# Kernel optimization log

Measured on AMD Instinct MI355X. Metric: run time of the kernel, lower is better.

The kernel has to match this reference:

```python
import jax, jax.numpy as jnp
import numpy as np
from jax import lax


def _pairwise_dist(a, b):
    # a: (T, D), b: (T, D) -> (T, T) Euclidean distances via GEMM trick
    a2 = jnp.sum(a * a, axis=-1)
    b2 = jnp.sum(b * b, axis=-1)
    sq = a2[:, None] + b2[None, :] - 2.0 * (a @ b.T)
    return jnp.sqrt(jnp.maximum(sq, 1e-12))


def _frechet(seq1, seq2):
    cost = _pairwise_dist(seq1, seq2)  # (T, T)
    ca0 = lax.cummax(cost[0])          # first row boundary: running max

    def row_step(prev, cost_row):
        # prev: ca[i-1, :]; cost_row: cost[i, :]
        c0 = jnp.maximum(prev[0], cost_row[0])  # first-column boundary

        def col_step(left, x):
            c, up, diag = x
            val = jnp.maximum(c, jnp.minimum(jnp.minimum(up, left), diag))
            return val, val

        _, rest = lax.scan(col_step, c0, (cost_row[1:], prev[1:], prev[:-1]))
        cur = jnp.concatenate([c0[None], rest])
        return cur, None

    final_row, _ = lax.scan(row_step, ca0, cost[1:])
    return final_row[-1]


def setup_inputs() -> dict:
    key = jax.random.key(0)
    k1, k2 = jax.random.split(key)
    B, T, D = 32, 1024, 64
    pred = jax.random.normal(k1, (B, T, D), dtype=jnp.float32)
    targ = jax.random.normal(k2, (B, T, D), dtype=jnp.float32)
    return {"pred": pred, "targ": targ}


def reference(pred, targ):
    dists = jax.vmap(_frechet)(pred, targ)  # (B,)
    return jnp.mean(dists)
```

## Files before the change

### kernel.cpp

```cpp
#include <hip/hip_runtime.h>
#include <hip/hip_bf16.h>

#define T_LEN 1024
#define D_DIM 64
#define BATCH 32

#define BM 64
#define BN 128

__global__ __launch_bounds__(256, 3) void cost_kernel(const float* __restrict__ pred,
                                                      const float* __restrict__ targ,
                                                      float* __restrict__ cost) {
    const int b = blockIdx.z;
    const float* P = pred + (size_t)b * T_LEN * D_DIM;
    const float* Tg = targ + (size_t)b * T_LEN * D_DIM;
    float* C = cost + (size_t)b * T_LEN * T_LEN;
    const int row0 = blockIdx.y * BM;
    const int col0 = blockIdx.x * BN;

    __shared__ __align__(16) float ps[BM][D_DIM + 4];
    __shared__ __align__(16) float ts[D_DIM][BN + 4];
    __shared__ float p2[BM], t2[BN];

    const int tid = threadIdx.x;

#pragma unroll
    for (int it = 0; it < 4; ++it) {
        int f = tid + 256 * it;
        int row = f >> 4;
        int kc = f & 15;
        float4 v = *(const float4*)(P + (size_t)(row0 + row) * D_DIM + 4 * kc);
        *(float4*)&ps[row][4 * kc] = v;
    }
#pragma unroll
    for (int it = 0; it < 8; ++it) {
        int f = tid + 256 * it;
        int col = f >> 4;
        int kc = f & 15;
        float4 w = *(const float4*)(Tg + (size_t)(col0 + col) * D_DIM + 4 * kc);
        ts[4 * kc + 0][col] = w.x;
        ts[4 * kc + 1][col] = w.y;
        ts[4 * kc + 2][col] = w.z;
        ts[4 * kc + 3][col] = w.w;
    }
    __syncthreads();

    if (tid < 64) {
        float s = 0.0f;
        const float4* pr = (const float4*)&ps[tid][0];
#pragma unroll
        for (int q = 0; q < 16; ++q) {
            float4 v = pr[q];
            s += v.x * v.x; s += v.y * v.y; s += v.z * v.z; s += v.w * v.w;
        }
        p2[tid] = s;
    } else if (tid < 192) {
        int c = tid - 64;
        float s = 0.0f;
#pragma unroll
        for (int k = 0; k < 64; ++k) { float x = ts[k][c]; s += x * x; }
        t2[c] = s;
    }
    __syncthreads();

    const int tx = tid & 31;
    const int ty = tid >> 5;
    const int r0 = 8 * ty, c0 = 4 * tx;

    float acc[8][4];
#pragma unroll
    for (int i = 0; i < 8; ++i)
#pragma unroll
        for (int j = 0; j < 4; ++j) acc[i][j] = 0.0f;

#pragma unroll
    for (int k4 = 0; k4 < 16; ++k4) {
        float4 b0 = *(const float4*)&ts[4 * k4 + 0][c0];
        float4 b1 = *(const float4*)&ts[4 * k4 + 1][c0];
        float4 b2 = *(const float4*)&ts[4 * k4 + 2][c0];
        float4 b3 = *(const float4*)&ts[4 * k4 + 3][c0];
#pragma unroll
        for (int i = 0; i < 8; ++i) {
            float4 a = *(const float4*)&ps[r0 + i][4 * k4];
            acc[i][0] += a.x * b0.x; acc[i][1] += a.x * b0.y; acc[i][2] += a.x * b0.z; acc[i][3] += a.x * b0.w;
            acc[i][0] += a.y * b1.x; acc[i][1] += a.y * b1.y; acc[i][2] += a.y * b1.z; acc[i][3] += a.y * b1.w;
            acc[i][0] += a.z * b2.x; acc[i][1] += a.z * b2.y; acc[i][2] += a.z * b2.z; acc[i][3] += a.z * b2.w;
            acc[i][0] += a.w * b3.x; acc[i][1] += a.w * b3.y; acc[i][2] += a.w * b3.z; acc[i][3] += a.w * b3.w;
        }
    }

    float4 tt = *(const float4*)&t2[c0];
#pragma unroll
    for (int i = 0; i < 8; ++i) {
        float pa = p2[r0 + i];
        float4 o;
        o.x = sqrtf(fmaxf(pa + tt.x - 2.0f * acc[i][0], 1e-12f));
        o.y = sqrtf(fmaxf(pa + tt.y - 2.0f * acc[i][1], 1e-12f));
        o.z = sqrtf(fmaxf(pa + tt.z - 2.0f * acc[i][2], 1e-12f));
        o.w = sqrtf(fmaxf(pa + tt.w - 2.0f * acc[i][3], 1e-12f));
        *(float4*)(C + (size_t)(row0 + r0 + i) * T_LEN + (col0 + c0)) = o;
    }
}

#define RD 12

__device__ __forceinline__ void gl_lds16(const float* g, void* l) {
    __builtin_amdgcn_global_load_lds(
        (const __attribute__((address_space(1))) unsigned int*)(const void*)g,
        (__attribute__((address_space(3))) unsigned int*)l, 16, 0, 0);
}

__device__ __forceinline__ float4 lds_read_b128(unsigned off) {
    float4 r;
    asm volatile("ds_read_b128 %0, %1" : "=v"(r) : "v"(off));
    return r;
}

__global__ __launch_bounds__(64) void dp_kernel(const float* __restrict__ cost,
                                                float* __restrict__ out) {
    const int b = blockIdx.x;
    const int t = threadIdx.x;
    const float INF = __builtin_inff();
    const float* C = cost + (size_t)b * T_LEN * T_LEN + 16 * t;

    __shared__ __align__(16) float4 ring[RD][4][64];

    const unsigned ring_base =
        (unsigned)(size_t)(__attribute__((address_space(3))) void*)&ring[0][0][0];
    const unsigned my_off = ring_base + 16u * (unsigned)t;

    float prev[16];
#pragma unroll
    for (int j = 0; j < 16; ++j) prev[j] = INF;
    float right_out = INF;
    float diag_feed = INF;

#pragma unroll
    for (int d = 0; d < RD; ++d) {
        int r = d - t; r = r < 0 ? 0 : (r > T_LEN - 1 ? T_LEN - 1 : r);
        const float* src = C + (size_t)r * T_LEN;
#pragma unroll
        for (int q = 0; q < 4; ++q) gl_lds16(src + 4 * q, &ring[d][q][0]);
    }

    float4 rA0, rA1, rA2, rA3, rB0, rB1, rB2, rB3;
    asm volatile("s_waitcnt vmcnt(44)" ::: "memory");
    __builtin_amdgcn_sched_barrier(0);
    rA0 = lds_read_b128(my_off + 0);
    rA1 = lds_read_b128(my_off + 1024);
    rA2 = lds_read_b128(my_off + 2048);
    rA3 = lds_read_b128(my_off + 3072);

    const int S = T_LEN + 63;
    const int NCH = (S + RD - 1) / RD;
    int s = 0;

#define DP_STEP(C0, C1, C2, C3, N0, N1, N2, N3, USLOT)                        \
    {                                                                         \
        asm volatile("s_waitcnt lgkmcnt(0)" ::: "memory");                    \
        __builtin_amdgcn_sched_barrier(0);                                    \
        const int r = s - t;                                                  \
        float inc = __shfl_up(right_out, 1, 64);                              \
        float left = inc, diag = diag_feed;                                   \
        diag_feed = inc;                                                      \
        if (t == 0) { left = (r == 0) ? -INF : INF; diag = INF; }             \
        if (r >= 0 && r < T_LEN) {                                            \
            float cb[16] = {C0.x, C0.y, C0.z, C0.w, C1.x, C1.y, C1.z, C1.w,   \
                            C2.x, C2.y, C2.z, C2.w, C3.x, C3.y, C3.z, C3.w};  \
            _Pragma("unroll")                                                 \
            for (int j = 0; j < 16; ++j) {                                    \
                float c = cb[j];                                              \
                float up = prev[j];                                           \
                float v = fmaxf(c, fminf(fminf(up, diag), left));             \
                diag = up; left = v; prev[j] = v;                             \
            }                                                                 \
            right_out = left;                                                 \
        }                                                                     \
        __builtin_amdgcn_sched_barrier(0);                                    \
        asm volatile("s_waitcnt vmcnt(40)" ::: "memory");                     \
        __builtin_amdgcn_sched_barrier(0);                                    \
        {                                                                     \
            const unsigned nb = my_off + ((((USLOT) + 1) % RD) * 4096u);      \
            N0 = lds_read_b128(nb + 0);                                       \
            N1 = lds_read_b128(nb + 1024);                                    \
            N2 = lds_read_b128(nb + 2048);                                    \
            N3 = lds_read_b128(nb + 3072);                                    \
            int rn = s + RD - t;                                              \
            rn = rn < 0 ? 0 : (rn > T_LEN - 1 ? T_LEN - 1 : rn);              \
            const float* src = C + (size_t)rn * T_LEN;                        \
            gl_lds16(src + 0,  &ring[USLOT][0][0]);                           \
            gl_lds16(src + 4,  &ring[USLOT][1][0]);                           \
            gl_lds16(src + 8,  &ring[USLOT][2][0]);                           \
            gl_lds16(src + 12, &ring[USLOT][3][0]);                           \
        }                                                                     \
        ++s;                                                                  \
    }

    for (int chunk = 0; chunk < NCH; ++chunk) {
        DP_STEP(rA0, rA1, rA2, rA3, rB0, rB1, rB2, rB3, 0)
        DP_STEP(rB0, rB1, rB2, rB3, rA0, rA1, rA2, rA3, 1)
        DP_STEP(rA0, rA1, rA2, rA3, rB0, rB1, rB2, rB3, 2)
        DP_STEP(rB0, rB1, rB2, rB3, rA0, rA1, rA2, rA3, 3)
        DP_STEP(rA0, rA1, rA2, rA3, rB0, rB1, rB2, rB3, 4)
        DP_STEP(rB0, rB1, rB2, rB3, rA0, rA1, rA2, rA3, 5)
        DP_STEP(rA0, rA1, rA2, rA3, rB0, rB1, rB2, rB3, 6)
        DP_STEP(rB0, rB1, rB2, rB3, rA0, rA1, rA2, rA3, 7)
        DP_STEP(rA0, rA1, rA2, rA3, rB0, rB1, rB2, rB3, 8)
        DP_STEP(rB0, rB1, rB2, rB3, rA0, rA1, rA2, rA3, 9)
        DP_STEP(rA0, rA1, rA2, rA3, rB0, rB1, rB2, rB3, 10)
        DP_STEP(rB0, rB1, rB2, rB3, rA0, rA1, rA2, rA3, 11)
    }
#undef DP_STEP

    asm volatile("s_waitcnt vmcnt(0) lgkmcnt(0)" ::: "memory");
    if (t == 63) atomicAdd(out, prev[15] * (1.0f / (float)BATCH));
}

__global__ __launch_bounds__(64) void dp_fused_kernel(const float* __restrict__ pred,
                                                      const float* __restrict__ targ,
                                                      float* __restrict__ out) {
    const int b = blockIdx.x;
    const int t = threadIdx.x;
    const float INF = __builtin_inff();
    const float* P = pred + (size_t)b * T_LEN * D_DIM;
    const float* T = targ + (size_t)b * T_LEN * D_DIM + (size_t)(16 * t) * D_DIM;

    float prev[16];
#pragma unroll
    for (int j = 0; j < 16; ++j) prev[j] = INF;
    float right_out = INF;
    float diag_feed = INF;

    for (int s = 0; s < T_LEN + 63; s++) {
        int r = s - t;
        float inc = __shfl_up(right_out, 1, 64);
        float left = inc, diag = diag_feed;
        diag_feed = inc;
        if (t == 0) { left = (r == 0) ? -INF : INF; diag = INF; }
        if (r >= 0 && r < T_LEN) {
            float4 pr[16];
            const float4* pp = (const float4*)(P + (size_t)r * D_DIM);
#pragma unroll
            for (int q = 0; q < 16; q++) pr[q] = pp[q];
#pragma unroll
            for (int j = 0; j < 16; j++) {
                const float4* tp = (const float4*)(T + (size_t)j * D_DIM);
                float acc = 0.0f;
#pragma unroll
                for (int q = 0; q < 16; q++) {
                    float4 tv = tp[q];
                    float dx = pr[q].x - tv.x; acc += dx * dx;
                    float dy = pr[q].y - tv.y; acc += dy * dy;
                    float dz = pr[q].z - tv.z; acc += dz * dz;
                    float dw = pr[q].w - tv.w; acc += dw * dw;
                }
                float c = sqrtf(fmaxf(acc, 1e-12f));
                float up = prev[j];
                float v = fmaxf(c, fminf(fminf(up, diag), left));
                diag = up; left = v; prev[j] = v;
            }
            right_out = left;
        }
    }
    if (t == 63) atomicAdd(out, prev[15] * (1.0f / (float)BATCH));
}

extern "C" void kernel_launch(void* const* d_in, const int* in_sizes, int n_in,
                              void* d_out, int out_size, void* d_ws, size_t ws_size,
                              hipStream_t stream) {
    const float* pred = (const float*)d_in[0];
    const float* targ = (const float*)d_in[1];
    float* out = (float*)d_out;

    hipMemsetAsync(out, 0, sizeof(float) * out_size, stream);

    const size_t per_batch = (size_t)T_LEN * T_LEN * sizeof(float);
    int bpg = (int)(ws_size / per_batch);
    if (bpg > BATCH) bpg = BATCH;

    if (bpg >= 1) {
        float* cost = (float*)d_ws;
        for (int g0 = 0; g0 < BATCH; g0 += bpg) {
            int gb = (BATCH - g0) < bpg ? (BATCH - g0) : bpg;
            dim3 grid(T_LEN / BN, T_LEN / BM, gb);
            cost_kernel<<<grid, 256, 0, stream>>>(pred + (size_t)g0 * T_LEN * D_DIM,
                                                  targ + (size_t)g0 * T_LEN * D_DIM,
                                                  cost);
            dp_kernel<<<gb, 64, 0, stream>>>(cost, out);
        }
    } else {
        dp_fused_kernel<<<BATCH, 64, 0, stream>>>(pred, targ, out);
    }
}
```

Baseline: 342.5 us.

## Replace LDS ring prefetch with register pipeline and med3-based DP recurrence

The DP kernel no longer stages cost rows through an LDS ring buffer via global_load_lds. It now keeps an 8-deep register pipeline of direct global_load_dwordx4 loads, waiting with vmcnt. The inner recurrence is also reformulated: the up/diag terms are precomputed independently, and the serial dependency on left becomes a single fmed3 per element, which shortens the critical chain. The register pipeline costs many VGPRs, and the shallower prefetch depth may expose more memory latency.

```diff
diff --git a/kernel.cpp b/kernel.cpp
--- a/kernel.cpp
+++ b/kernel.cpp
@@ -102,19 +102,15 @@
     }
 }
 
-#define RD 12
-
-__device__ __forceinline__ void gl_lds16(const float* g, void* l) {
-    __builtin_amdgcn_global_load_lds(
-        (const __attribute__((address_space(1))) unsigned int*)(const void*)g,
-        (__attribute__((address_space(3))) unsigned int*)l, 16, 0, 0);
-}
-
-__device__ __forceinline__ float4 lds_read_b128(unsigned off) {
-    float4 r;
-    asm volatile("ds_read_b128 %0, %1" : "=v"(r) : "v"(off));
-    return r;
-}
+#define PD 8
+
+#define DP_LOAD4(D0, D1, D2, D3, SRC)                                         \
+    asm volatile("global_load_dwordx4 %0, %4, off\n\t"                        \
+                 "global_load_dwordx4 %1, %4, off offset:16\n\t"              \
+                 "global_load_dwordx4 %2, %4, off offset:32\n\t"              \
+                 "global_load_dwordx4 %3, %4, off offset:48"                  \
+                 : "=&v"(D0), "=&v"(D1), "=&v"(D2), "=&v"(D3)                 \
+                 : "v"(SRC))
 
 __global__ __launch_bounds__(64) void dp_kernel(const float* __restrict__ cost,
                                                 float* __restrict__ out) {
@@ -123,96 +119,76 @@
     const float INF = __builtin_inff();
     const float* C = cost + (size_t)b * T_LEN * T_LEN + 16 * t;
 
-    __shared__ __align__(16) float4 ring[RD][4][64];
-
-    const unsigned ring_base =
-        (unsigned)(size_t)(__attribute__((address_space(3))) void*)&ring[0][0][0];
-    const unsigned my_off = ring_base + 16u * (unsigned)t;
-
     float prev[16];
 #pragma unroll
     for (int j = 0; j < 16; ++j) prev[j] = INF;
     float right_out = INF;
     float diag_feed = INF;
 
-#pragma unroll
-    for (int d = 0; d < RD; ++d) {
+    float4 pipe[PD][4];
+
+#pragma unroll
+    for (int d = 0; d < PD; ++d) {
         int r = d - t; r = r < 0 ? 0 : (r > T_LEN - 1 ? T_LEN - 1 : r);
         const float* src = C + (size_t)r * T_LEN;
-#pragma unroll
-        for (int q = 0; q < 4; ++q) gl_lds16(src + 4 * q, &ring[d][q][0]);
-    }
-
-    float4 rA0, rA1, rA2, rA3, rB0, rB1, rB2, rB3;
-    asm volatile("s_waitcnt vmcnt(44)" ::: "memory");
-    __builtin_amdgcn_sched_barrier(0);
-    rA0 = lds_read_b128(my_off + 0);
-    rA1 = lds_read_b128(my_off + 1024);
-    rA2 = lds_read_b128(my_off + 2048);
-    rA3 = lds_read_b128(my_off + 3072);
+        DP_LOAD4(pipe[d][0], pipe[d][1], pipe[d][2], pipe[d][3], src);
+    }
 
     const int S = T_LEN + 63;
-    const int NCH = (S + RD - 1) / RD;
+    const int NCH = (S + PD - 1) / PD;
     int s = 0;
 
-#define DP_STEP(C0, C1, C2, C3, N0, N1, N2, N3, USLOT)                        \
+#define DP_STEP(U)                                                            \
     {                                                                         \
-        asm volatile("s_waitcnt lgkmcnt(0)" ::: "memory");                    \
+           \
+        asm volatile("s_waitcnt vmcnt(28)" ::: "memory");                     \
         __builtin_amdgcn_sched_barrier(0);                                    \
+        const float4 q0 = pipe[U][0], q1 = pipe[U][1];                        \
+        const float4 q2 = pipe[U][2], q3 = pipe[U][3];                        \
         const int r = s - t;                                                  \
         float inc = __shfl_up(right_out, 1, 64);                              \
         float left = inc, diag = diag_feed;                                   \
         diag_feed = inc;                                                      \
         if (t == 0) { left = (r == 0) ? -INF : INF; diag = INF; }             \
         if (r >= 0 && r < T_LEN) {                                            \
-            float cb[16] = {C0.x, C0.y, C0.z, C0.w, C1.x, C1.y, C1.z, C1.w,   \
-                            C2.x, C2.y, C2.z, C2.w, C3.x, C3.y, C3.z, C3.w};  \
+            float cq[16] = {q0.x, q0.y, q0.z, q0.w, q1.x, q1.y, q1.z, q1.w,   \
+                            q2.x, q2.y, q2.z, q2.w, q3.x, q3.y, q3.z, q3.w};  \
+            float g[16];                                                      \
+            g[0] = fmaxf(cq[0], fminf(prev[0], diag));                        \
+            _Pragma("unroll")                                                 \
+            for (int j = 1; j < 16; ++j)                                      \
+                g[j] = fmaxf(cq[j], fminf(prev[j], prev[j - 1]));             \
+            float v = left;                                                   \
             _Pragma("unroll")                                                 \
             for (int j = 0; j < 16; ++j) {                                    \
-                float c = cb[j];                                              \
-                float up = prev[j];                                           \
-                float v = fmaxf(c, fminf(fminf(up, diag), left));             \
-                diag = up; left = v; prev[j] = v;                             \
+                v = __builtin_amdgcn_fmed3f(v, cq[j], g[j]);                  \
+                prev[j] = v;                                                  \
             }                                                                 \
-            right_out = left;                                                 \
+            right_out = v;                                                    \
         }                                                                     \
         __builtin_amdgcn_sched_barrier(0);                                    \
-        asm volatile("s_waitcnt vmcnt(40)" ::: "memory");                     \
-        __builtin_amdgcn_sched_barrier(0);                                    \
         {                                                                     \
-            const unsigned nb = my_off + ((((USLOT) + 1) % RD) * 4096u);      \
-            N0 = lds_read_b128(nb + 0);                                       \
-            N1 = lds_read_b128(nb + 1024);                                    \
-            N2 = lds_read_b128(nb + 2048);                                    \
-            N3 = lds_read_b128(nb + 3072);                                    \
-            int rn = s + RD - t;                                              \
+            int rn = s + PD - t;                                              \
             rn = rn < 0 ? 0 : (rn > T_LEN - 1 ? T_LEN - 1 : rn);              \
             const float* src = C + (size_t)rn * T_LEN;                        \
-            gl_lds16(src + 0,  &ring[USLOT][0][0]);                           \
-            gl_lds16(src + 4,  &ring[USLOT][1][0]);                           \
-            gl_lds16(src + 8,  &ring[USLOT][2][0]);                           \
-            gl_lds16(src + 12, &ring[USLOT][3][0]);                           \
+            DP_LOAD4(pipe[U][0], pipe[U][1], pipe[U][2], pipe[U][3], src);    \
         }                                                                     \
         ++s;                                                                  \
     }
 
     for (int chunk = 0; chunk < NCH; ++chunk) {
-        DP_STEP(rA0, rA1, rA2, rA3, rB0, rB1, rB2, rB3, 0)
-        DP_STEP(rB0, rB1, rB2, rB3, rA0, rA1, rA2, rA3, 1)
-        DP_STEP(rA0, rA1, rA2, rA3, rB0, rB1, rB2, rB3, 2)
-        DP_STEP(rB0, rB1, rB2, rB3, rA0, rA1, rA2, rA3, 3)
-        DP_STEP(rA0, rA1, rA2, rA3, rB0, rB1, rB2, rB3, 4)
-        DP_STEP(rB0, rB1, rB2, rB3, rA0, rA1, rA2, rA3, 5)
-        DP_STEP(rA0, rA1, rA2, rA3, rB0, rB1, rB2, rB3, 6)
-        DP_STEP(rB0, rB1, rB2, rB3, rA0, rA1, rA2, rA3, 7)
-        DP_STEP(rA0, rA1, rA2, rA3, rB0, rB1, rB2, rB3, 8)
-        DP_STEP(rB0, rB1, rB2, rB3, rA0, rA1, rA2, rA3, 9)
-        DP_STEP(rA0, rA1, rA2, rA3, rB0, rB1, rB2, rB3, 10)
-        DP_STEP(rB0, rB1, rB2, rB3, rA0, rA1, rA2, rA3, 11)
+        DP_STEP(0)
+        DP_STEP(1)
+        DP_STEP(2)
+        DP_STEP(3)
+        DP_STEP(4)
+        DP_STEP(5)
+        DP_STEP(6)
+        DP_STEP(7)
     }
 #undef DP_STEP
 
-    asm volatile("s_waitcnt vmcnt(0) lgkmcnt(0)" ::: "memory");
+    asm volatile("s_waitcnt vmcnt(0)" ::: "memory");
     if (t == 63) atomicAdd(out, prev[15] * (1.0f / (float)BATCH));
 }
 
```

Measured after the change: 360.1 us. 1.05x slower.
